# Optimization experiments

Hardware: AMD Instinct MI355X
Metric: run time of the kernel (lower is better)

Reference implementation:

```python
import jax, jax.numpy as jnp
import numpy as np

B, S, H = 8, 2048, 768

def setup_inputs() -> dict:
    key = jax.random.key(0)
    ks = jax.random.split(key, 11)
    queries = jax.random.normal(ks[0], (B, S, H), dtype=jnp.float32)
    keys_ = jax.random.normal(ks[1], (B, S, H), dtype=jnp.float32)
    values = jax.random.normal(ks[2], (B, S, H), dtype=jnp.float32)
    coordinates = jax.random.uniform(ks[3], (B, S, 2), dtype=jnp.float32)
    scale = 1.0 / np.sqrt(H)
    Wq = jax.random.normal(ks[4], (H, H), dtype=jnp.float32) * scale
    bq = jnp.zeros((H,), dtype=jnp.float32)
    Wk = jax.random.normal(ks[5], (H, H), dtype=jnp.float32) * scale
    bk = jnp.zeros((H,), dtype=jnp.float32)
    Wv = jax.random.normal(ks[6], (H, H), dtype=jnp.float32) * scale
    bv = jnp.zeros((H,), dtype=jnp.float32)
    spatial_weight = jax.random.normal(ks[7], (1,), dtype=jnp.float32)
    return {"queries": queries, "keys": keys_, "values": values,
            "coordinates": coordinates, "Wq": Wq, "bq": bq, "Wk": Wk,
            "bk": bk, "Wv": Wv, "bv": bv, "spatial_weight": spatial_weight}

def _cdist(c):
    # c: [B, S, 2] -> pairwise euclidean distances [B, S, S]
    sq = jnp.sum(c * c, axis=-1)  # [B, S]
    d2 = sq[:, :, None] + sq[:, None, :] - 2.0 * jnp.einsum('bsd,btd->bst', c, c)
    return jnp.sqrt(jnp.maximum(d2, 1e-12))

def reference(queries, keys, values, coordinates, Wq, bq, Wk, bk, Wv, bv, spatial_weight):
    q = queries @ Wq.T + bq  # [B, S, H]
    k = keys @ Wk.T + bk
    v = values @ Wv.T + bv
    scores = jnp.einsum('bsh,bth->bst', q, k)          # [B, S, S]
    scores = scores - spatial_weight[0] * _cdist(coordinates)
    attn = jax.nn.softmax(scores, axis=-1)
    out = jnp.einsum('bst,bth->bsh', attn, v)          # [B, S, H]
    return out, attn
```

## Files before the change

kernel.cpp:

```cpp
#include <hip/hip_runtime.h>
#include <stdint.h>


typedef _Float16 half8 __attribute__((ext_vector_type(8)));
typedef _Float16 half4v __attribute__((ext_vector_type(4)));
typedef float f32x4 __attribute__((ext_vector_type(4)));

#define DEVI static __device__ __forceinline__

constexpr int B_ = 8, S_ = 2048, H_ = 768;
constexpr long NX = (long)B_ * S_ * H_;
constexpr long NW = (long)H_ * H_;

DEVI void glds16(const void* g, void* l) {
  __builtin_amdgcn_global_load_lds(
      (const __attribute__((address_space(1))) uint32_t*)g,
      (__attribute__((address_space(3))) uint32_t*)l, 16, 0, 0);
}

DEVI void stage_tile(const _Float16* gbase, int rowStride, _Float16* lds, int tid) {
#pragma unroll
  for (int seg = 0; seg < 2; ++seg) {
    int u = seg * 256 + tid;
    int r = u >> 2, c = u & 3;
    int sc = c ^ ((r >> 1) & 3);
    glds16(gbase + (long)r * rowStride + sc * 8, lds + ((u & ~63) << 3));
  }
}

DEVI half8 frag(const _Float16* lds, int m0, int lane) {
  int row = m0 + (lane & 15);
  int c = (lane >> 4) ^ ((row >> 1) & 3);
  return *(const half8*)(lds + row * 32 + c * 8);
}

__global__ __launch_bounds__(256) void k_split(
    const float* __restrict__ xq, const float* __restrict__ xk,
    const float* __restrict__ xv, const float* __restrict__ wq,
    const float* __restrict__ wk, const float* __restrict__ wv,
    _Float16* __restrict__ dst) {
  const long NX4 = NX / 4, NW4 = NW / 4, TOT = 3 * NX4 + 3 * NW4;
  for (long u = (long)blockIdx.x * blockDim.x + threadIdx.x; u < TOT;
       u += (long)gridDim.x * blockDim.x) {
    const float4* src;
    _Float16 *dh, *dl;
    long idx;
    if (u < 3 * NX4) {
      int z = (u >= 2 * NX4) ? 2 : (u >= NX4) ? 1 : 0;
      idx = u - (long)z * NX4;
      src = (const float4*)(z == 0 ? xq : z == 1 ? xk : xv);
      dh = dst + (long)z * 2 * NX;
      dl = dh + NX;
    } else {
      long t = u - 3 * NX4;
      int z = (t >= 2 * NW4) ? 2 : (t >= NW4) ? 1 : 0;
      idx = t - (long)z * NW4;
      src = (const float4*)(z == 0 ? wq : z == 1 ? wk : wv);
      dh = dst + 6 * NX + (long)z * 2 * NW;
      dl = dh + NW;
    }
    float4 x = src[idx];
    half4v hi, lo;
    hi[0] = (_Float16)x.x; lo[0] = (_Float16)(x.x - (float)hi[0]);
    hi[1] = (_Float16)x.y; lo[1] = (_Float16)(x.y - (float)hi[1]);
    hi[2] = (_Float16)x.z; lo[2] = (_Float16)(x.z - (float)hi[2]);
    hi[3] = (_Float16)x.w; lo[3] = (_Float16)(x.w - (float)hi[3]);
    *(half4v*)(dh + idx * 4) = hi;
    *(half4v*)(dl + idx * 4) = lo;
  }
}

__global__ __launch_bounds__(256, 2) void k_proj(
    const _Float16* __restrict__ scratch, const float* __restrict__ bq,
    const float* __restrict__ bk, const float* __restrict__ bv,
    _Float16* __restrict__ qh, _Float16* __restrict__ ql,
    _Float16* __restrict__ kh, _Float16* __restrict__ kl,
    _Float16* __restrict__ vT) {
  const int nt = blockIdx.x, mt = blockIdx.y, z = blockIdx.z;
  const int tid = threadIdx.x;
  const bool full = (z < 2);
  const _Float16* Xh = scratch + (long)z * 2 * NX;
  const _Float16* Xl = Xh + NX;
  const _Float16* Wh = scratch + 6 * NX + (long)z * 2 * NW;
  const _Float16* Wl = Wh + NW;
  const float* bias = (z == 0) ? bq : (z == 1) ? bk : bv;

  __shared__ _Float16 sm[2][4][4096];

  f32x4 acc[4][4] = {};

  const _Float16* Ah = Xh + (long)(mt * 128) * H_;
  const _Float16* Al = Xl + (long)(mt * 128) * H_;
  const _Float16* Bh = Wh + (long)(nt * 128) * H_;
  const _Float16* Bl = Wl + (long)(nt * 128) * H_;

  stage_tile(Ah, H_, sm[0][0], tid);
  stage_tile(Bh, H_, sm[0][2], tid);
  if (full) {
    stage_tile(Al, H_, sm[0][1], tid);
    stage_tile(Bl, H_, sm[0][3], tid);
  }
  __syncthreads();

  const int lane = tid & 63, wid = tid >> 6;
  const int wm = (wid >> 1) * 64, wn = (wid & 1) * 64;

  int cur = 0;
  for (int kk = 0; kk < 24; ++kk) {
    if (kk + 1 < 24) {
      int o = (kk + 1) * 32;
      stage_tile(Ah + o, H_, sm[cur ^ 1][0], tid);
      stage_tile(Bh + o, H_, sm[cur ^ 1][2], tid);
      if (full) {
        stage_tile(Al + o, H_, sm[cur ^ 1][1], tid);
        stage_tile(Bl + o, H_, sm[cur ^ 1][3], tid);
      }
    }
    half8 ah[4], bh[4];
#pragma unroll
    for (int i = 0; i < 4; ++i) ah[i] = frag(sm[cur][0], wm + i * 16, lane);
#pragma unroll
    for (int j = 0; j < 4; ++j) bh[j] = frag(sm[cur][2], wn + j * 16, lane);
#pragma unroll
    for (int i = 0; i < 4; ++i)
#pragma unroll
      for (int j = 0; j < 4; ++j)
        acc[i][j] = __builtin_amdgcn_mfma_f32_16x16x32_f16(ah[i], bh[j],
                                                           acc[i][j], 0, 0, 0);
    if (full) {
      half8 al[4], bl[4];
#pragma unroll
      for (int i = 0; i < 4; ++i) al[i] = frag(sm[cur][1], wm + i * 16, lane);
#pragma unroll
      for (int j = 0; j < 4; ++j) bl[j] = frag(sm[cur][3], wn + j * 16, lane);
#pragma unroll
      for (int i = 0; i < 4; ++i)
#pragma unroll
        for (int j = 0; j < 4; ++j) {
          acc[i][j] = __builtin_amdgcn_mfma_f32_16x16x32_f16(ah[i], bl[j],
                                                             acc[i][j], 0, 0, 0);
          acc[i][j] = __builtin_amdgcn_mfma_f32_16x16x32_f16(al[i], bh[j],
                                                             acc[i][j], 0, 0, 0);
        }
    }
    __syncthreads();
    cur ^= 1;
  }

  _Float16* oh = (z == 0) ? qh : kh;
  _Float16* ol = (z == 0) ? ql : kl;
#pragma unroll
  for (int i = 0; i < 4; ++i) {
    int m_t = wm + i * 16 + ((lane >> 4) << 2);
#pragma unroll
    for (int j = 0; j < 4; ++j) {
      int n_t = wn + j * 16 + (lane & 15);
      int gn = nt * 128 + n_t;
      float bs = bias[gn];
      if (z < 2) {
#pragma unroll
        for (int r = 0; r < 4; ++r) {
          long gm = (long)mt * 128 + m_t + r;
          float y = acc[i][j][r] + bs;
          _Float16 hi = (_Float16)y;
          oh[gm * H_ + gn] = hi;
          ol[gm * H_ + gn] = (_Float16)(y - (float)hi);
        }
      } else {
        int gmI = mt * 128 + m_t;
        int bb = gmI >> 11, t0 = gmI & 2047;
        half4v pk;
#pragma unroll
        for (int r = 0; r < 4; ++r) pk[r] = (_Float16)(acc[i][j][r] + bs);
        *(half4v*)&vT[((long)bb * H_ + gn) * S_ + t0] = pk;
      }
    }
  }
}

__global__ __launch_bounds__(256, 2) void k_scores(
    const _Float16* __restrict__ qh, const _Float16* __restrict__ ql,
    const _Float16* __restrict__ kh, const _Float16* __restrict__ kl,
    const float* __restrict__ coords, const float* __restrict__ sw,
    float* __restrict__ attn) {
  const int nt = blockIdx.x, mt = blockIdx.y, b = blockIdx.z;
  const int tid = threadIdx.x;
  __shared__ _Float16 sm[2][4][4096];
  __shared__ float cr[2][128], cc[2][128];

  if (tid < 128) {
    long gi = (long)b * S_ + mt * 128 + tid;
    cr[0][tid] = coords[gi * 2 + 0];
    cr[1][tid] = coords[gi * 2 + 1];
  } else {
    int t = tid - 128;
    long gj = (long)b * S_ + nt * 128 + t;
    cc[0][t] = coords[gj * 2 + 0];
    cc[1][t] = coords[gj * 2 + 1];
  }
  const float w = sw[0];

  f32x4 acc[4][4] = {};
  const long aoff = ((long)b * S_ + mt * 128) * H_;
  const long boff = ((long)b * S_ + nt * 128) * H_;
  const _Float16* Ah = qh + aoff;
  const _Float16* Al = ql + aoff;
  const _Float16* Bh = kh + boff;
  const _Float16* Bl = kl + boff;

  stage_tile(Ah, H_, sm[0][0], tid);
  stage_tile(Al, H_, sm[0][1], tid);
  stage_tile(Bh, H_, sm[0][2], tid);
  stage_tile(Bl, H_, sm[0][3], tid);
  __syncthreads();

  const int lane = tid & 63, wid = tid >> 6;
  const int wm = (wid >> 1) * 64, wn = (wid & 1) * 64;

  int cur = 0;
  for (int kk = 0; kk < 24; ++kk) {
    if (kk + 1 < 24) {
      int o = (kk + 1) * 32;
      stage_tile(Ah + o, H_, sm[cur ^ 1][0], tid);
      stage_tile(Al + o, H_, sm[cur ^ 1][1], tid);
      stage_tile(Bh + o, H_, sm[cur ^ 1][2], tid);
      stage_tile(Bl + o, H_, sm[cur ^ 1][3], tid);
    }
    half8 ah[4], al4[4], bh[4], bl4[4];
#pragma unroll
    for (int i = 0; i < 4; ++i) {
      ah[i] = frag(sm[cur][0], wm + i * 16, lane);
      al4[i] = frag(sm[cur][1], wm + i * 16, lane);
    }
#pragma unroll
    for (int j = 0; j < 4; ++j) {
      bh[j] = frag(sm[cur][2], wn + j * 16, lane);
      bl4[j] = frag(sm[cur][3], wn + j * 16, lane);
    }
#pragma unroll
    for (int i = 0; i < 4; ++i)
#pragma unroll
      for (int j = 0; j < 4; ++j) {
        acc[i][j] = __builtin_amdgcn_mfma_f32_16x16x32_f16(ah[i], bh[j],
                                                           acc[i][j], 0, 0, 0);
        acc[i][j] = __builtin_amdgcn_mfma_f32_16x16x32_f16(ah[i], bl4[j],
                                                           acc[i][j], 0, 0, 0);
        acc[i][j] = __builtin_amdgcn_mfma_f32_16x16x32_f16(al4[i], bh[j],
                                                           acc[i][j], 0, 0, 0);
      }
    __syncthreads();
    cur ^= 1;
  }

#pragma unroll
  for (int i = 0; i < 4; ++i) {
    int m_t = wm + i * 16 + ((lane >> 4) << 2);
#pragma unroll
    for (int j = 0; j < 4; ++j) {
      int n_t = wn + j * 16 + (lane & 15);
      float cjx = cc[0][n_t], cjy = cc[1][n_t];
      long rowbase = ((long)b * S_ + mt * 128 + m_t) * S_ + nt * 128 + n_t;
#pragma unroll
      for (int r = 0; r < 4; ++r) {
        float dx = cr[0][m_t + r] - cjx;
        float dy = cr[1][m_t + r] - cjy;
        float d = sqrtf(fmaxf(fmaf(dx, dx, dy * dy), 1e-12f));
        attn[rowbase + (long)r * S_] = acc[i][j][r] - w * d;
      }
    }
  }
}

__global__ __launch_bounds__(256) void k_rowsoft(float* __restrict__ attn) {
  const int wid = threadIdx.x >> 6, lane = threadIdx.x & 63;
  float* p = attn + ((long)blockIdx.x * 4 + wid) * S_;
  float4 v[8];
#pragma unroll
  for (int i = 0; i < 8; ++i) v[i] = ((const float4*)p)[i * 64 + lane];
  float m = -3.4e38f;
#pragma unroll
  for (int i = 0; i < 8; ++i)
    m = fmaxf(m, fmaxf(fmaxf(v[i].x, v[i].y), fmaxf(v[i].z, v[i].w)));
#pragma unroll
  for (int o = 32; o > 0; o >>= 1) m = fmaxf(m, __shfl_xor(m, o));
  float l = 0.f;
#pragma unroll
  for (int i = 0; i < 8; ++i) {
    v[i].x = __expf(v[i].x - m);
    v[i].y = __expf(v[i].y - m);
    v[i].z = __expf(v[i].z - m);
    v[i].w = __expf(v[i].w - m);
    l += (v[i].x + v[i].y) + (v[i].z + v[i].w);
  }
#pragma unroll
  for (int o = 32; o > 0; o >>= 1) l += __shfl_xor(l, o);
  const float rl = 1.0f / l;
#pragma unroll
  for (int i = 0; i < 8; ++i) {
    v[i].x *= rl; v[i].y *= rl; v[i].z *= rl; v[i].w *= rl;
    ((float4*)p)[i * 64 + lane] = v[i];
  }
}

__global__ __launch_bounds__(256, 2) void k_pv(
    const float* __restrict__ attn, const _Float16* __restrict__ vT,
    float* __restrict__ outp) {
  const int nt = blockIdx.x, mt = blockIdx.y, b = blockIdx.z;
  const int tid = threadIdx.x;
  __shared__ _Float16 sm[2][2][4096];
  f32x4 acc[4][4] = {};
  const float* Ab = attn + ((long)b * S_ + mt * 128) * S_;
  const _Float16* Bb = vT + ((long)b * H_ + nt * 128) * S_;
  const int lane = tid & 63, wid = tid >> 6;
  const int wm = (wid >> 1) * 64, wn = (wid & 1) * 64;

  stage_tile(Bb, S_, sm[0][1], tid);
#pragma unroll
  for (int seg = 0; seg < 2; ++seg) {
    int u = seg * 256 + tid, r = u >> 2, c = u & 3;
    int sc = c ^ ((r >> 1) & 3);
    const float4* s4 = (const float4*)(Ab + (long)r * S_ + sc * 8);
    float4 x0 = s4[0], x1 = s4[1];
    half8 h = {(_Float16)x0.x, (_Float16)x0.y, (_Float16)x0.z, (_Float16)x0.w,
               (_Float16)x1.x, (_Float16)x1.y, (_Float16)x1.z, (_Float16)x1.w};
    *(half8*)(&sm[0][0][r * 32 + c * 8]) = h;
  }
  __syncthreads();

  int cur = 0;
  for (int kk = 0; kk < 64; ++kk) {
    float4 x0a, x1a, x0b, x1b;
    const bool pre = (kk + 1 < 64);
    if (pre) {
      stage_tile(Bb + (kk + 1) * 32, S_, sm[cur ^ 1][1], tid);
      {
        int u = tid, r = u >> 2, sc = (u & 3) ^ ((r >> 1) & 3);
        const float4* s4 =
            (const float4*)(Ab + (long)r * S_ + (kk + 1) * 32 + sc * 8);
        x0a = s4[0]; x1a = s4[1];
      }
      {
        int u = 256 + tid, r = u >> 2, sc = (u & 3) ^ ((r >> 1) & 3);
        const float4* s4 =
            (const float4*)(Ab + (long)r * S_ + (kk + 1) * 32 + sc * 8);
        x0b = s4[0]; x1b = s4[1];
      }
    }
    half8 ah[4], bh[4];
#pragma unroll
    for (int i = 0; i < 4; ++i) ah[i] = frag(sm[cur][0], wm + i * 16, lane);
#pragma unroll
    for (int j = 0; j < 4; ++j) bh[j] = frag(sm[cur][1], wn + j * 16, lane);
#pragma unroll
    for (int i = 0; i < 4; ++i)
#pragma unroll
      for (int j = 0; j < 4; ++j)
        acc[i][j] = __builtin_amdgcn_mfma_f32_16x16x32_f16(ah[i], bh[j],
                                                           acc[i][j], 0, 0, 0);
    if (pre) {
      {
        int u = tid, r = u >> 2, c = u & 3;
        half8 h = {(_Float16)x0a.x, (_Float16)x0a.y, (_Float16)x0a.z,
                   (_Float16)x0a.w, (_Float16)x1a.x, (_Float16)x1a.y,
                   (_Float16)x1a.z, (_Float16)x1a.w};
        *(half8*)(&sm[cur ^ 1][0][r * 32 + c * 8]) = h;
      }
      {
        int u = 256 + tid, r = u >> 2, c = u & 3;
        half8 h = {(_Float16)x0b.x, (_Float16)x0b.y, (_Float16)x0b.z,
                   (_Float16)x0b.w, (_Float16)x1b.x, (_Float16)x1b.y,
                   (_Float16)x1b.z, (_Float16)x1b.w};
        *(half8*)(&sm[cur ^ 1][0][r * 32 + c * 8]) = h;
      }
    }
    __syncthreads();
    cur ^= 1;
  }

#pragma unroll
  for (int i = 0; i < 4; ++i) {
    int m_t = wm + i * 16 + ((lane >> 4) << 2);
#pragma unroll
    for (int j = 0; j < 4; ++j) {
      int n_t = wn + j * 16 + (lane & 15);
      int h = nt * 128 + n_t;
      long rowbase = (long)b * S_ + mt * 128 + m_t;
#pragma unroll
      for (int r = 0; r < 4; ++r) outp[(rowbase + r) * H_ + h] = acc[i][j][r];
    }
  }
}

extern "C" void kernel_launch(void* const* d_in, const int* in_sizes, int n_in,
                              void* d_out, int out_size, void* d_ws,
                              size_t ws_size, hipStream_t stream) {
  const float* xq = (const float*)d_in[0];
  const float* xk = (const float*)d_in[1];
  const float* xv = (const float*)d_in[2];
  const float* co = (const float*)d_in[3];
  const float* wq = (const float*)d_in[4];
  const float* bq = (const float*)d_in[5];
  const float* wk = (const float*)d_in[6];
  const float* bk = (const float*)d_in[7];
  const float* wv = (const float*)d_in[8];
  const float* bv = (const float*)d_in[9];
  const float* sw = (const float*)d_in[10];

  float* out = (float*)d_out;
  float* attn = out + NX;
  _Float16* scratch = (_Float16*)d_out;

  _Float16* qh = (_Float16*)d_ws;
  _Float16* ql = qh + NX;
  _Float16* kh = ql + NX;
  _Float16* kl = kh + NX;
  _Float16* vT = kl + NX;

  k_split<<<dim3(2048), 256, 0, stream>>>(xq, xk, xv, wq, wk, wv, scratch);
  k_proj<<<dim3(6, 128, 3), 256, 0, stream>>>(scratch, bq, bk, bv, qh, ql, kh,
                                              kl, vT);
  k_scores<<<dim3(16, 16, 8), 256, 0, stream>>>(qh, ql, kh, kl, co, sw, attn);
  k_rowsoft<<<dim3(4096), 256, 0, stream>>>(attn);
  k_pv<<<dim3(6, 16, 8), 256, 0, stream>>>(attn, vT, out);
}
```

Measured before the change: 557.8 us.

## Rewrite scores GEMM with 256x256 tiles and a 4-stage async LDS pipeline

The QK^T scores kernel now uses 512-thread blocks computing 256x256 output tiles. The three split-precision products (hi*hi, hi*lo, lo*hi) are flattened into one 72-step K loop that stages only two operand tiles per step. A 4-deep ring of LDS buffers is filled with global_load_lds, using swizzled offsets, explicit vmcnt waits and raw barriers, and MFMA runs at raised priority. The aim is more reuse per loaded byte and better overlap of loads with matrix math. The cost is far fewer blocks (512) and heavier register and LDS use per block, which may limit occupancy.

```diff
diff --git a/kernel.cpp b/kernel.cpp
--- a/kernel.cpp
+++ b/kernel.cpp
@@ -178,88 +178,126 @@
   }
 }
 
-__global__ __launch_bounds__(256, 2) void k_scores(
+__global__ __launch_bounds__(512, 2) void k_scores2(
     const _Float16* __restrict__ qh, const _Float16* __restrict__ ql,
     const _Float16* __restrict__ kh, const _Float16* __restrict__ kl,
     const float* __restrict__ coords, const float* __restrict__ sw,
     float* __restrict__ attn) {
   const int nt = blockIdx.x, mt = blockIdx.y, b = blockIdx.z;
   const int tid = threadIdx.x;
-  __shared__ _Float16 sm[2][4][4096];
-  __shared__ float cr[2][128], cc[2][128];
-
-  if (tid < 128) {
-    long gi = (long)b * S_ + mt * 128 + tid;
+  const int lane = tid & 63, wid = tid >> 6;
+  const int wr = wid >> 2, wc = wid & 3;
+
+  __shared__ _Float16 lds[4][2][8192];
+  __shared__ float cr[2][256], cc[2][256];
+
+  if (tid < 256) {
+    long gi = (long)b * S_ + mt * 256 + tid;
     cr[0][tid] = coords[gi * 2 + 0];
     cr[1][tid] = coords[gi * 2 + 1];
   } else {
-    int t = tid - 128;
-    long gj = (long)b * S_ + nt * 128 + t;
+    int t = tid - 256;
+    long gj = (long)b * S_ + nt * 256 + t;
     cc[0][t] = coords[gj * 2 + 0];
     cc[1][t] = coords[gj * 2 + 1];
   }
   const float w = sw[0];
 
-  f32x4 acc[4][4] = {};
-  const long aoff = ((long)b * S_ + mt * 128) * H_;
-  const long boff = ((long)b * S_ + nt * 128) * H_;
-  const _Float16* Ah = qh + aoff;
-  const _Float16* Al = ql + aoff;
-  const _Float16* Bh = kh + boff;
-  const _Float16* Bl = kl + boff;
-
-  stage_tile(Ah, H_, sm[0][0], tid);
-  stage_tile(Al, H_, sm[0][1], tid);
-  stage_tile(Bh, H_, sm[0][2], tid);
-  stage_tile(Bl, H_, sm[0][3], tid);
-  __syncthreads();
-
-  const int lane = tid & 63, wid = tid >> 6;
-  const int wm = (wid >> 1) * 64, wn = (wid & 1) * 64;
-
-  int cur = 0;
-  for (int kk = 0; kk < 24; ++kk) {
-    if (kk + 1 < 24) {
-      int o = (kk + 1) * 32;
-      stage_tile(Ah + o, H_, sm[cur ^ 1][0], tid);
-      stage_tile(Al + o, H_, sm[cur ^ 1][1], tid);
-      stage_tile(Bh + o, H_, sm[cur ^ 1][2], tid);
-      stage_tile(Bl + o, H_, sm[cur ^ 1][3], tid);
-    }
-    half8 ah[4], al4[4], bh[4], bl4[4];
-#pragma unroll
-    for (int i = 0; i < 4; ++i) {
-      ah[i] = frag(sm[cur][0], wm + i * 16, lane);
-      al4[i] = frag(sm[cur][1], wm + i * 16, lane);
-    }
+  const long aoff = ((long)b * S_ + mt * 256) * H_;
+  const long boff = ((long)b * S_ + nt * 256) * H_;
+
+  long goff[2];
+  int loff[2];
+#pragma unroll
+  for (int seg = 0; seg < 2; ++seg) {
+    int u = seg * 512 + tid;
+    int r = u >> 2, c = u & 3;
+    int sc = c ^ ((r >> 1) & 3);
+    goff[seg] = (long)r * H_ + sc * 8;
+    loff[seg] = (u & ~63) << 3;
+  }
+
+  f32x4 acc[8][4] = {};
+
+  auto asrc = [&](int kt) -> const _Float16* {
+    int term = kt / 24, ko = (kt % 24) * 32;
+    return (term == 2 ? ql : qh) + aoff + ko;
+  };
+  auto bsrc = [&](int kt) -> const _Float16* {
+    int term = kt / 24, ko = (kt % 24) * 32;
+    return (term == 1 ? kl : kh) + boff + ko;
+  };
+  auto stage_tile4 = [&](int kt) {
+    const _Float16* sa = asrc(kt);
+    const _Float16* sb = bsrc(kt);
+    _Float16* la = &lds[kt & 3][0][0];
+    _Float16* lb = &lds[kt & 3][1][0];
+    glds16(sa + goff[0], la + loff[0]);
+    glds16(sa + goff[1], la + loff[1]);
+    glds16(sb + goff[0], lb + loff[0]);
+    glds16(sb + goff[1], lb + loff[1]);
+  };
+
+  auto compute = [&](int kt, const _Float16* sa, const _Float16* sb, bool st) {
+    const _Float16* A = &lds[kt & 3][0][0];
+    const _Float16* Bt = &lds[kt & 3][1][0];
+    _Float16* nla = &lds[(kt + 3) & 3][0][0];
+    _Float16* nlb = &lds[(kt + 3) & 3][1][0];
+#pragma unroll
+    for (int q = 0; q < 4; ++q) {
+      const int mh = q >> 1, nh = q & 1;
+      if (st) {
+        int seg = q & 1;
+        if (q < 2)
+          glds16(sa + goff[seg], nla + loff[seg]);
+        else
+          glds16(sb + goff[seg], nlb + loff[seg]);
+      }
+      half8 af[4], bf[2];
+#pragma unroll
+      for (int i = 0; i < 4; ++i)
+        af[i] = frag(A, wr * 128 + (mh * 4 + i) * 16, lane);
+#pragma unroll
+      for (int j = 0; j < 2; ++j)
+        bf[j] = frag(Bt, wc * 64 + (nh * 2 + j) * 16, lane);
+      __builtin_amdgcn_s_setprio(1);
+#pragma unroll
+      for (int i = 0; i < 4; ++i)
+#pragma unroll
+        for (int j = 0; j < 2; ++j)
+          acc[mh * 4 + i][nh * 2 + j] = __builtin_amdgcn_mfma_f32_16x16x32_f16(
+              af[i], bf[j], acc[mh * 4 + i][nh * 2 + j], 0, 0, 0);
+      __builtin_amdgcn_s_setprio(0);
+    }
+  };
+
+  stage_tile4(0);
+  stage_tile4(1);
+  stage_tile4(2);
+  asm volatile("s_waitcnt vmcnt(8)" ::: "memory");
+  __builtin_amdgcn_s_barrier();
+
+  for (int kt = 0; kt < 69; ++kt) {
+    compute(kt, asrc(kt + 3), bsrc(kt + 3), true);
+    asm volatile("s_waitcnt vmcnt(8)" ::: "memory");
+    __builtin_amdgcn_s_barrier();
+  }
+  compute(69, nullptr, nullptr, false);
+  asm volatile("s_waitcnt vmcnt(4)" ::: "memory");
+  __builtin_amdgcn_s_barrier();
+  compute(70, nullptr, nullptr, false);
+  asm volatile("s_waitcnt vmcnt(0)" ::: "memory");
+  __builtin_amdgcn_s_barrier();
+  compute(71, nullptr, nullptr, false);
+
+#pragma unroll
+  for (int i = 0; i < 8; ++i) {
+    int m_t = wr * 128 + i * 16 + ((lane >> 4) << 2);
 #pragma unroll
     for (int j = 0; j < 4; ++j) {
-      bh[j] = frag(sm[cur][2], wn + j * 16, lane);
-      bl4[j] = frag(sm[cur][3], wn + j * 16, lane);
-    }
-#pragma unroll
-    for (int i = 0; i < 4; ++i)
-#pragma unroll
-      for (int j = 0; j < 4; ++j) {
-        acc[i][j] = __builtin_amdgcn_mfma_f32_16x16x32_f16(ah[i], bh[j],
-                                                           acc[i][j], 0, 0, 0);
-        acc[i][j] = __builtin_amdgcn_mfma_f32_16x16x32_f16(ah[i], bl4[j],
-                                                           acc[i][j], 0, 0, 0);
-        acc[i][j] = __builtin_amdgcn_mfma_f32_16x16x32_f16(al4[i], bh[j],
-                                                           acc[i][j], 0, 0, 0);
-      }
-    __syncthreads();
-    cur ^= 1;
-  }
-
-#pragma unroll
-  for (int i = 0; i < 4; ++i) {
-    int m_t = wm + i * 16 + ((lane >> 4) << 2);
-#pragma unroll
-    for (int j = 0; j < 4; ++j) {
-      int n_t = wn + j * 16 + (lane & 15);
+      int n_t = wc * 64 + j * 16 + (lane & 15);
       float cjx = cc[0][n_t], cjy = cc[1][n_t];
-      long rowbase = ((long)b * S_ + mt * 128 + m_t) * S_ + nt * 128 + n_t;
+      long rowbase = ((long)b * S_ + mt * 256 + m_t) * S_ + nt * 256 + n_t;
 #pragma unroll
       for (int r = 0; r < 4; ++r) {
         float dx = cr[0][m_t + r] - cjx;
@@ -419,7 +457,7 @@
   k_split<<<dim3(2048), 256, 0, stream>>>(xq, xk, xv, wq, wk, wv, scratch);
   k_proj<<<dim3(6, 128, 3), 256, 0, stream>>>(scratch, bq, bk, bv, qh, ql, kh,
                                               kl, vT);
-  k_scores<<<dim3(16, 16, 8), 256, 0, stream>>>(qh, ql, kh, kl, co, sw, attn);
+  k_scores2<<<dim3(8, 8, 8), 512, 0, stream>>>(qh, ql, kh, kl, co, sw, attn);
   k_rowsoft<<<dim3(4096), 256, 0, stream>>>(attn);
   k_pv<<<dim3(6, 16, 8), 256, 0, stream>>>(attn, vT, out);
 }
```

New measurement: 616.3 us. 10.5% more time.

## Fold Wq and Wk into one matrix so only one activation projection is needed

Applied to the files above, without the earlier changes.

Rewrites the scores as (Xq·(Wq^T Wk))·Xk^T plus rank-one bias terms. A small GEMM builds G = Wq^T Wk, only Xq is projected by it, and the raw Xk is used directly as the key operand. This drops one full 16K×768×768 split-precision projection. The per-row and per-column bias corrections are added in the scores epilogue. The value projection now runs straight from fp32 in its own kernel. Softmax also writes an fp16 copy of the attention matrix so the PV GEMM can stage it with direct global-to-LDS loads. The cost is extra small kernels, a 2048×2048×8 fp16 write, and numerical drift from the reassociated product.

```diff
diff --git a/kernel.cpp b/kernel.cpp
--- a/kernel.cpp
+++ b/kernel.cpp
@@ -11,6 +11,7 @@
 constexpr int B_ = 8, S_ = 2048, H_ = 768;
 constexpr long NX = (long)B_ * S_ * H_;
 constexpr long NW = (long)H_ * H_;
+constexpr long ATT = (long)B_ * S_ * S_;
 
 DEVI void glds16(const void* g, void* l) {
   __builtin_amdgcn_global_load_lds(
@@ -34,30 +35,49 @@
   return *(const half8*)(lds + row * 32 + c * 8);
 }
 
+__global__ __launch_bounds__(128) void k_uv(const float* __restrict__ wq,
+                                            const float* __restrict__ wk,
+                                            const float* __restrict__ bq,
+                                            const float* __restrict__ bk,
+                                            float* u, float* vv, float* cb) {
+  int i = blockIdx.x * 128 + threadIdx.x;
+  if (blockIdx.y == 0) {
+    float a = 0;
+    for (int j = 0; j < H_; ++j) a += wq[(long)j * H_ + i] * bk[j];
+    u[i] = a;
+    if (i == 0) {
+      float c = 0;
+      for (int j = 0; j < H_; ++j) c += bq[j] * bk[j];
+      cb[0] = c;
+    }
+  } else {
+    float a = 0;
+    for (int j = 0; j < H_; ++j) a += wk[(long)j * H_ + i] * bq[j];
+    vv[i] = a;
+  }
+}
+
 __global__ __launch_bounds__(256) void k_split(
     const float* __restrict__ xq, const float* __restrict__ xk,
-    const float* __restrict__ xv, const float* __restrict__ wq,
-    const float* __restrict__ wk, const float* __restrict__ wv,
-    _Float16* __restrict__ dst) {
-  const long NX4 = NX / 4, NW4 = NW / 4, TOT = 3 * NX4 + 3 * NW4;
-  for (long u = (long)blockIdx.x * blockDim.x + threadIdx.x; u < TOT;
-       u += (long)gridDim.x * blockDim.x) {
+    const float* __restrict__ wq, const float* __restrict__ wk,
+    _Float16* __restrict__ xh, _Float16* __restrict__ xl,
+    _Float16* __restrict__ yh, _Float16* __restrict__ yl,
+    _Float16* __restrict__ wqh, _Float16* __restrict__ wql,
+    _Float16* __restrict__ wkh, _Float16* __restrict__ wkl) {
+  const long NX4 = NX / 4, NW4 = NW / 4, TOT = 2 * NX4 + 2 * NW4;
+  for (long t = (long)blockIdx.x * blockDim.x + threadIdx.x; t < TOT;
+       t += (long)gridDim.x * blockDim.x) {
     const float4* src;
     _Float16 *dh, *dl;
     long idx;
-    if (u < 3 * NX4) {
-      int z = (u >= 2 * NX4) ? 2 : (u >= NX4) ? 1 : 0;
-      idx = u - (long)z * NX4;
-      src = (const float4*)(z == 0 ? xq : z == 1 ? xk : xv);
-      dh = dst + (long)z * 2 * NX;
-      dl = dh + NX;
+    if (t < NX4) {
+      src = (const float4*)xq; dh = xh; dl = xl; idx = t;
+    } else if (t < 2 * NX4) {
+      src = (const float4*)xk; dh = yh; dl = yl; idx = t - NX4;
     } else {
-      long t = u - 3 * NX4;
-      int z = (t >= 2 * NW4) ? 2 : (t >= NW4) ? 1 : 0;
-      idx = t - (long)z * NW4;
-      src = (const float4*)(z == 0 ? wq : z == 1 ? wk : wv);
-      dh = dst + 6 * NX + (long)z * 2 * NW;
-      dl = dh + NW;
+      long v = t - 2 * NX4;
+      if (v < NW4) { src = (const float4*)wq; dh = wqh; dl = wql; idx = v; }
+      else { src = (const float4*)wk; dh = wkh; dl = wkl; idx = v - NW4; }
     }
     float4 x = src[idx];
     half4v hi, lo;
@@ -70,36 +90,67 @@
   }
 }
 
-__global__ __launch_bounds__(256, 2) void k_proj(
-    const _Float16* __restrict__ scratch, const float* __restrict__ bq,
-    const float* __restrict__ bk, const float* __restrict__ bv,
-    _Float16* __restrict__ qh, _Float16* __restrict__ ql,
-    _Float16* __restrict__ kh, _Float16* __restrict__ kl,
-    _Float16* __restrict__ vT) {
-  const int nt = blockIdx.x, mt = blockIdx.y, z = blockIdx.z;
+__global__ __launch_bounds__(256) void k_tr(const _Float16* __restrict__ in,
+                                            _Float16* __restrict__ out) {
+  const int z = blockIdx.z;
+  const _Float16* src = in + (long)z * NW;
+  _Float16* dst = out + (long)z * NW;
+  __shared__ _Float16 t[64][72];
+  int r0 = blockIdx.y * 64, c0 = blockIdx.x * 64;
+#pragma unroll
+  for (int it = 0; it < 2; ++it) {
+    int idx = it * 256 + threadIdx.x;
+    int r = idx >> 3, ch = idx & 7;
+    *(half8*)&t[r][ch * 8] = *(const half8*)(src + (long)(r0 + r) * H_ + c0 + ch * 8);
+  }
+  __syncthreads();
+#pragma unroll
+  for (int it = 0; it < 2; ++it) {
+    int idx = it * 256 + threadIdx.x;
+    int r = idx >> 3, ch = idx & 7;
+    half8 v;
+#pragma unroll
+    for (int k = 0; k < 8; ++k) v[k] = t[ch * 8 + k][r];
+    *(half8*)(dst + (long)(c0 + r) * H_ + r0 + ch * 8) = v;
+  }
+}
+
+__global__ __launch_bounds__(256) void k_dot(const float* __restrict__ src,
+                                             const float* __restrict__ vec,
+                                             const float* __restrict__ cb,
+                                             float* __restrict__ dst, int addc) {
+  int wid = threadIdx.x >> 6, lane = threadIdx.x & 63;
+  long row = (long)blockIdx.x * 4 + wid;
+  const float4* p = (const float4*)(src + row * H_);
+  const float4* q = (const float4*)vec;
+  float s = 0;
+#pragma unroll
+  for (int k = 0; k < 3; ++k) {
+    float4 a = p[lane + k * 64], b = q[lane + k * 64];
+    s += a.x * b.x + a.y * b.y + a.z * b.z + a.w * b.w;
+  }
+#pragma unroll
+  for (int o = 32; o; o >>= 1) s += __shfl_xor(s, o);
+  if (lane == 0) dst[row] = s + (addc ? cb[0] : 0.0f);
+}
+
+__global__ __launch_bounds__(256, 2) void k_gemm3(
+    const _Float16* __restrict__ Ah_, const _Float16* __restrict__ Al_,
+    const _Float16* __restrict__ Bh_, const _Float16* __restrict__ Bl_,
+    _Float16* __restrict__ Oh, _Float16* __restrict__ Ol) {
+  const int nt = blockIdx.x, mt = blockIdx.y;
   const int tid = threadIdx.x;
-  const bool full = (z < 2);
-  const _Float16* Xh = scratch + (long)z * 2 * NX;
-  const _Float16* Xl = Xh + NX;
-  const _Float16* Wh = scratch + 6 * NX + (long)z * 2 * NW;
-  const _Float16* Wl = Wh + NW;
-  const float* bias = (z == 0) ? bq : (z == 1) ? bk : bv;
-
   __shared__ _Float16 sm[2][4][4096];
-
   f32x4 acc[4][4] = {};
-
-  const _Float16* Ah = Xh + (long)(mt * 128) * H_;
-  const _Float16* Al = Xl + (long)(mt * 128) * H_;
-  const _Float16* Bh = Wh + (long)(nt * 128) * H_;
-  const _Float16* Bl = Wl + (long)(nt * 128) * H_;
+  const _Float16* Ah = Ah_ + (long)(mt * 128) * H_;
+  const _Float16* Al = Al_ + (long)(mt * 128) * H_;
+  const _Float16* Bh = Bh_ + (long)(nt * 128) * H_;
+  const _Float16* Bl = Bl_ + (long)(nt * 128) * H_;
 
   stage_tile(Ah, H_, sm[0][0], tid);
   stage_tile(Bh, H_, sm[0][2], tid);
-  if (full) {
-    stage_tile(Al, H_, sm[0][1], tid);
-    stage_tile(Bl, H_, sm[0][3], tid);
-  }
+  stage_tile(Al, H_, sm[0][1], tid);
+  stage_tile(Bl, H_, sm[0][3], tid);
   __syncthreads();
 
   const int lane = tid & 63, wid = tid >> 6;
@@ -111,44 +162,35 @@
       int o = (kk + 1) * 32;
       stage_tile(Ah + o, H_, sm[cur ^ 1][0], tid);
       stage_tile(Bh + o, H_, sm[cur ^ 1][2], tid);
-      if (full) {
-        stage_tile(Al + o, H_, sm[cur ^ 1][1], tid);
-        stage_tile(Bl + o, H_, sm[cur ^ 1][3], tid);
+      stage_tile(Al + o, H_, sm[cur ^ 1][1], tid);
+      stage_tile(Bl + o, H_, sm[cur ^ 1][3], tid);
+    }
+    half8 ah[4], bh[4], al[4], bl[4];
+#pragma unroll
+    for (int i = 0; i < 4; ++i) {
+      ah[i] = frag(sm[cur][0], wm + i * 16, lane);
+      al[i] = frag(sm[cur][1], wm + i * 16, lane);
+    }
+#pragma unroll
+    for (int j = 0; j < 4; ++j) {
+      bh[j] = frag(sm[cur][2], wn + j * 16, lane);
+      bl[j] = frag(sm[cur][3], wn + j * 16, lane);
+    }
+#pragma unroll
+    for (int i = 0; i < 4; ++i)
+#pragma unroll
+      for (int j = 0; j < 4; ++j) {
+        acc[i][j] = __builtin_amdgcn_mfma_f32_16x16x32_f16(ah[i], bh[j],
+                                                           acc[i][j], 0, 0, 0);
+        acc[i][j] = __builtin_amdgcn_mfma_f32_16x16x32_f16(ah[i], bl[j],
+                                                           acc[i][j], 0, 0, 0);
+        acc[i][j] = __builtin_amdgcn_mfma_f32_16x16x32_f16(al[i], bh[j],
+                                                           acc[i][j], 0, 0, 0);
       }
-    }
-    half8 ah[4], bh[4];
-#pragma unroll
-    for (int i = 0; i < 4; ++i) ah[i] = frag(sm[cur][0], wm + i * 16, lane);
-#pragma unroll
-    for (int j = 0; j < 4; ++j) bh[j] = frag(sm[cur][2], wn + j * 16, lane);
-#pragma unroll
-    for (int i = 0; i < 4; ++i)
-#pragma unroll
-      for (int j = 0; j < 4; ++j)
-        acc[i][j] = __builtin_amdgcn_mfma_f32_16x16x32_f16(ah[i], bh[j],
-                                                           acc[i][j], 0, 0, 0);
-    if (full) {
-      half8 al[4], bl[4];
-#pragma unroll
-      for (int i = 0; i < 4; ++i) al[i] = frag(sm[cur][1], wm + i * 16, lane);
-#pragma unroll
-      for (int j = 0; j < 4; ++j) bl[j] = frag(sm[cur][3], wn + j * 16, lane);
-#pragma unroll
-      for (int i = 0; i < 4; ++i)
-#pragma unroll
-        for (int j = 0; j < 4; ++j) {
-          acc[i][j] = __builtin_amdgcn_mfma_f32_16x16x32_f16(ah[i], bl[j],
-                                                             acc[i][j], 0, 0, 0);
-          acc[i][j] = __builtin_amdgcn_mfma_f32_16x16x32_f16(al[i], bh[j],
-                                                             acc[i][j], 0, 0, 0);
-        }
-    }
     __syncthreads();
     cur ^= 1;
   }
 
-  _Float16* oh = (z == 0) ? qh : kh;
-  _Float16* ol = (z == 0) ? ql : kl;
 #pragma unroll
   for (int i = 0; i < 4; ++i) {
     int m_t = wm + i * 16 + ((lane >> 4) << 2);
@@ -156,57 +198,50 @@
     for (int j = 0; j < 4; ++j) {
       int n_t = wn + j * 16 + (lane & 15);
       int gn = nt * 128 + n_t;
-      float bs = bias[gn];
-      if (z < 2) {
-#pragma unroll
-        for (int r = 0; r < 4; ++r) {
-          long gm = (long)mt * 128 + m_t + r;
-          float y = acc[i][j][r] + bs;
-          _Float16 hi = (_Float16)y;
-          oh[gm * H_ + gn] = hi;
-          ol[gm * H_ + gn] = (_Float16)(y - (float)hi);
-        }
-      } else {
-        int gmI = mt * 128 + m_t;
-        int bb = gmI >> 11, t0 = gmI & 2047;
-        half4v pk;
-#pragma unroll
-        for (int r = 0; r < 4; ++r) pk[r] = (_Float16)(acc[i][j][r] + bs);
-        *(half4v*)&vT[((long)bb * H_ + gn) * S_ + t0] = pk;
+#pragma unroll
+      for (int r = 0; r < 4; ++r) {
+        long gm = (long)mt * 128 + m_t + r;
+        float y = acc[i][j][r];
+        _Float16 hi = (_Float16)y;
+        Oh[gm * H_ + gn] = hi;
+        Ol[gm * H_ + gn] = (_Float16)(y - (float)hi);
       }
     }
   }
 }
 
 __global__ __launch_bounds__(256, 2) void k_scores(
-    const _Float16* __restrict__ qh, const _Float16* __restrict__ ql,
-    const _Float16* __restrict__ kh, const _Float16* __restrict__ kl,
+    const _Float16* __restrict__ ph, const _Float16* __restrict__ pl,
+    const _Float16* __restrict__ yh, const _Float16* __restrict__ yl,
     const float* __restrict__ coords, const float* __restrict__ sw,
+    const float* __restrict__ rowadd, const float* __restrict__ coladd,
     float* __restrict__ attn) {
   const int nt = blockIdx.x, mt = blockIdx.y, b = blockIdx.z;
   const int tid = threadIdx.x;
   __shared__ _Float16 sm[2][4][4096];
-  __shared__ float cr[2][128], cc[2][128];
+  __shared__ float cr[2][128], cc[2][128], ra[128], ca[128];
 
   if (tid < 128) {
     long gi = (long)b * S_ + mt * 128 + tid;
     cr[0][tid] = coords[gi * 2 + 0];
     cr[1][tid] = coords[gi * 2 + 1];
+    ra[tid] = rowadd[gi];
   } else {
     int t = tid - 128;
     long gj = (long)b * S_ + nt * 128 + t;
     cc[0][t] = coords[gj * 2 + 0];
     cc[1][t] = coords[gj * 2 + 1];
+    ca[t] = coladd[gj];
   }
   const float w = sw[0];
 
   f32x4 acc[4][4] = {};
   const long aoff = ((long)b * S_ + mt * 128) * H_;
   const long boff = ((long)b * S_ + nt * 128) * H_;
-  const _Float16* Ah = qh + aoff;
-  const _Float16* Al = ql + aoff;
-  const _Float16* Bh = kh + boff;
-  const _Float16* Bl = kl + boff;
+  const _Float16* Ah = ph + aoff;
+  const _Float16* Al = pl + aoff;
+  const _Float16* Bh = yh + boff;
+  const _Float16* Bl = yl + boff;
 
   stage_tile(Ah, H_, sm[0][0], tid);
   stage_tile(Al, H_, sm[0][1], tid);
@@ -265,15 +300,18 @@
         float dx = cr[0][m_t + r] - cjx;
         float dy = cr[1][m_t + r] - cjy;
         float d = sqrtf(fmaxf(fmaf(dx, dx, dy * dy), 1e-12f));
-        attn[rowbase + (long)r * S_] = acc[i][j][r] - w * d;
+        attn[rowbase + (long)r * S_] = acc[i][j][r] - w * d + ra[m_t + r] + ca[n_t];
       }
     }
   }
 }
 
-__global__ __launch_bounds__(256) void k_rowsoft(float* __restrict__ attn) {
+__global__ __launch_bounds__(256) void k_rowsoft(float* __restrict__ attn,
+                                                 _Float16* __restrict__ a16) {
   const int wid = threadIdx.x >> 6, lane = threadIdx.x & 63;
-  float* p = attn + ((long)blockIdx.x * 4 + wid) * S_;
+  long row = (long)blockIdx.x * 4 + wid;
+  float* p = attn + row * S_;
+  _Float16* p16 = a16 + row * S_;
   float4 v[8];
 #pragma unroll
   for (int i = 0; i < 8; ++i) v[i] = ((const float4*)p)[i * 64 + lane];
@@ -299,52 +337,122 @@
   for (int i = 0; i < 8; ++i) {
     v[i].x *= rl; v[i].y *= rl; v[i].z *= rl; v[i].w *= rl;
     ((float4*)p)[i * 64 + lane] = v[i];
-  }
-}
-
-__global__ __launch_bounds__(256, 2) void k_pv(
-    const float* __restrict__ attn, const _Float16* __restrict__ vT,
+    half4v h = {(_Float16)v[i].x, (_Float16)v[i].y, (_Float16)v[i].z,
+                (_Float16)v[i].w};
+    ((half4v*)p16)[i * 64 + lane] = h;
+  }
+}
+
+__global__ __launch_bounds__(256, 2) void k_projv(
+    const float* __restrict__ vals, const float* __restrict__ wv,
+    const float* __restrict__ bv, _Float16* __restrict__ vT) {
+  const int nt = blockIdx.x, mt = blockIdx.y;
+  const int tid = threadIdx.x, lane = tid & 63, wid = tid >> 6;
+  const int wm = (wid >> 1) * 64, wn = (wid & 1) * 64;
+  __shared__ _Float16 sm[2][2][4096];
+  f32x4 acc[4][4] = {};
+  const float* Ab = vals + (long)(mt * 128) * H_;
+  const float* Bb = wv + (long)(nt * 128) * H_;
+
+#pragma unroll
+  for (int op = 0; op < 2; ++op) {
+    const float* gb = op ? Bb : Ab;
+#pragma unroll
+    for (int seg = 0; seg < 2; ++seg) {
+      int u = seg * 256 + tid, r = u >> 2, c = u & 3;
+      int sc = c ^ ((r >> 1) & 3);
+      const float4* s4 = (const float4*)(gb + (long)r * H_ + sc * 8);
+      float4 x0 = s4[0], x1 = s4[1];
+      half8 h = {(_Float16)x0.x, (_Float16)x0.y, (_Float16)x0.z, (_Float16)x0.w,
+                 (_Float16)x1.x, (_Float16)x1.y, (_Float16)x1.z, (_Float16)x1.w};
+      *(half8*)(&sm[0][op][r * 32 + c * 8]) = h;
+    }
+  }
+  __syncthreads();
+
+  int cur = 0;
+  for (int kk = 0; kk < 24; ++kk) {
+    float4 pa[2][2], pb[2][2];
+    const bool pre = (kk + 1 < 24);
+    if (pre) {
+#pragma unroll
+      for (int seg = 0; seg < 2; ++seg) {
+        int u = seg * 256 + tid, r = u >> 2;
+        int sc = (u & 3) ^ ((r >> 1) & 3);
+        const float4* s4 = (const float4*)(Ab + (long)r * H_ + (kk + 1) * 32 + sc * 8);
+        pa[seg][0] = s4[0]; pa[seg][1] = s4[1];
+        const float4* t4 = (const float4*)(Bb + (long)r * H_ + (kk + 1) * 32 + sc * 8);
+        pb[seg][0] = t4[0]; pb[seg][1] = t4[1];
+      }
+    }
+    half8 ah[4], bh[4];
+#pragma unroll
+    for (int i = 0; i < 4; ++i) ah[i] = frag(sm[cur][0], wm + i * 16, lane);
+#pragma unroll
+    for (int j = 0; j < 4; ++j) bh[j] = frag(sm[cur][1], wn + j * 16, lane);
+#pragma unroll
+    for (int i = 0; i < 4; ++i)
+#pragma unroll
+      for (int j = 0; j < 4; ++j)
+        acc[i][j] = __builtin_amdgcn_mfma_f32_16x16x32_f16(ah[i], bh[j],
+                                                           acc[i][j], 0, 0, 0);
+    if (pre) {
+#pragma unroll
+      for (int op = 0; op < 2; ++op) {
+#pragma unroll
+        for (int seg = 0; seg < 2; ++seg) {
+          int u = seg * 256 + tid, r = u >> 2, c = u & 3;
+          float4 x0 = op ? pb[seg][0] : pa[seg][0];
+          float4 x1 = op ? pb[seg][1] : pa[seg][1];
+          half8 h = {(_Float16)x0.x, (_Float16)x0.y, (_Float16)x0.z,
+                     (_Float16)x0.w, (_Float16)x1.x, (_Float16)x1.y,
+                     (_Float16)x1.z, (_Float16)x1.w};
+          *(half8*)(&sm[cur ^ 1][op][r * 32 + c * 8]) = h;
+        }
+      }
+    }
+    __syncthreads();
+    cur ^= 1;
+  }
+
+#pragma unroll
+  for (int i = 0; i < 4; ++i) {
+    int m_t = wm + i * 16 + ((lane >> 4) << 2);
+#pragma unroll
+    for (int j = 0; j < 4; ++j) {
+      int n_t = wn + j * 16 + (lane & 15);
+      int gn = nt * 128 + n_t;
+      float bs = bv[gn];
+      int gmI = mt * 128 + m_t;
+      int bb = gmI >> 11, t0 = gmI & 2047;
+      half4v pk;
+#pragma unroll
+      for (int r = 0; r < 4; ++r) pk[r] = (_Float16)(acc[i][j][r] + bs);
+      *(half4v*)&vT[((long)bb * H_ + gn) * S_ + t0] = pk;
+    }
+  }
+}
+
+__global__ __launch_bounds__(256, 2) void k_pv16(
+    const _Float16* __restrict__ a16, const _Float16* __restrict__ vT,
     float* __restrict__ outp) {
   const int nt = blockIdx.x, mt = blockIdx.y, b = blockIdx.z;
-  const int tid = threadIdx.x;
+  const int tid = threadIdx.x, lane = tid & 63, wid = tid >> 6;
+  const int wm = (wid >> 1) * 64, wn = (wid & 1) * 64;
   __shared__ _Float16 sm[2][2][4096];
   f32x4 acc[4][4] = {};
-  const float* Ab = attn + ((long)b * S_ + mt * 128) * S_;
+  const _Float16* Ab = a16 + ((long)b * S_ + mt * 128) * S_;
   const _Float16* Bb = vT + ((long)b * H_ + nt * 128) * S_;
-  const int lane = tid & 63, wid = tid >> 6;
-  const int wm = (wid >> 1) * 64, wn = (wid & 1) * 64;
-
+
+  stage_tile(Ab, S_, sm[0][0], tid);
   stage_tile(Bb, S_, sm[0][1], tid);
-#pragma unroll
-  for (int seg = 0; seg < 2; ++seg) {
-    int u = seg * 256 + tid, r = u >> 2, c = u & 3;
-    int sc = c ^ ((r >> 1) & 3);
-    const float4* s4 = (const float4*)(Ab + (long)r * S_ + sc * 8);
-    float4 x0 = s4[0], x1 = s4[1];
-    half8 h = {(_Float16)x0.x, (_Float16)x0.y, (_Float16)x0.z, (_Float16)x0.w,
-               (_Float16)x1.x, (_Float16)x1.y, (_Float16)x1.z, (_Float16)x1.w};
-    *(half8*)(&sm[0][0][r * 32 + c * 8]) = h;
-  }
   __syncthreads();
 
   int cur = 0;
   for (int kk = 0; kk < 64; ++kk) {
-    float4 x0a, x1a, x0b, x1b;
-    const bool pre = (kk + 1 < 64);
-    if (pre) {
+    if (kk + 1 < 64) {
+      stage_tile(Ab + (kk + 1) * 32, S_, sm[cur ^ 1][0], tid);
       stage_tile(Bb + (kk + 1) * 32, S_, sm[cur ^ 1][1], tid);
-      {
-        int u = tid, r = u >> 2, sc = (u & 3) ^ ((r >> 1) & 3);
-        const float4* s4 =
-            (const float4*)(Ab + (long)r * S_ + (kk + 1) * 32 + sc * 8);
-        x0a = s4[0]; x1a = s4[1];
-      }
-      {
-        int u = 256 + tid, r = u >> 2, sc = (u & 3) ^ ((r >> 1) & 3);
-        const float4* s4 =
-            (const float4*)(Ab + (long)r * S_ + (kk + 1) * 32 + sc * 8);
-        x0b = s4[0]; x1b = s4[1];
-      }
     }
     half8 ah[4], bh[4];
 #pragma unroll
@@ -357,22 +465,6 @@
       for (int j = 0; j < 4; ++j)
         acc[i][j] = __builtin_amdgcn_mfma_f32_16x16x32_f16(ah[i], bh[j],
                                                            acc[i][j], 0, 0, 0);
-    if (pre) {
-      {
-        int u = tid, r = u >> 2, c = u & 3;
-        half8 h = {(_Float16)x0a.x, (_Float16)x0a.y, (_Float16)x0a.z,
-                   (_Float16)x0a.w, (_Float16)x1a.x, (_Float16)x1a.y,
-                   (_Float16)x1a.z, (_Float16)x1a.w};
-        *(half8*)(&sm[cur ^ 1][0][r * 32 + c * 8]) = h;
-      }
-      {
-        int u = 256 + tid, r = u >> 2, c = u & 3;
-        half8 h = {(_Float16)x0b.x, (_Float16)x0b.y, (_Float16)x0b.z,
-                   (_Float16)x0b.w, (_Float16)x1b.x, (_Float16)x1b.y,
-                   (_Float16)x1b.z, (_Float16)x1b.w};
-        *(half8*)(&sm[cur ^ 1][0][r * 32 + c * 8]) = h;
-      }
-    }
     __syncthreads();
     cur ^= 1;
   }
@@ -408,18 +500,41 @@
 
   float* out = (float*)d_out;
   float* attn = out + NX;
-  _Float16* scratch = (_Float16*)d_out;
-
-  _Float16* qh = (_Float16*)d_ws;
-  _Float16* ql = qh + NX;
-  _Float16* kh = ql + NX;
-  _Float16* kl = kh + NX;
-  _Float16* vT = kl + NX;
-
-  k_split<<<dim3(2048), 256, 0, stream>>>(xq, xk, xv, wq, wk, wv, scratch);
-  k_proj<<<dim3(6, 128, 3), 256, 0, stream>>>(scratch, bq, bk, bv, qh, ql, kh,
-                                              kl, vT);
-  k_scores<<<dim3(16, 16, 8), 256, 0, stream>>>(qh, ql, kh, kl, co, sw, attn);
-  k_rowsoft<<<dim3(4096), 256, 0, stream>>>(attn);
-  k_pv<<<dim3(6, 16, 8), 256, 0, stream>>>(attn, vT, out);
-}
+
+  _Float16* sc = (_Float16*)d_out;
+  _Float16* Xh = sc;
+  _Float16* Xl = sc + NX;
+  _Float16* Wbase = sc + 2 * NX;
+  _Float16* WT = Wbase + 4 * NW;
+  _Float16* GtH = Wbase + 8 * NW;
+  _Float16* GtL = GtH + NW;
+
+  _Float16* wsh = (_Float16*)d_ws;
+  _Float16* Ph = wsh;
+  _Float16* Pl = wsh + NX;
+  _Float16* Yh = wsh + 2 * NX;
+  _Float16* Yl = wsh + 3 * NX;
+  float* extras = (float*)(wsh + 4 * NX);
+  float* rowadd = extras;
+  float* coladd = extras + 16384;
+  float* u = extras + 32768;
+  float* vv = u + H_;
+  float* cb = vv + H_;
+  _Float16* a16 = wsh;
+  _Float16* vT = wsh + ATT;
+
+  k_uv<<<dim3(6, 2), 128, 0, stream>>>(wq, wk, bq, bk, u, vv, cb);
+  k_split<<<2048, 256, 0, stream>>>(xq, xk, wq, wk, Xh, Xl, Yh, Yl, Wbase,
+                                    Wbase + NW, Wbase + 2 * NW, Wbase + 3 * NW);
+  k_tr<<<dim3(12, 12, 4), 256, 0, stream>>>(Wbase, WT);
+  k_gemm3<<<dim3(6, 6), 256, 0, stream>>>(WT + 2 * NW, WT + 3 * NW, WT,
+                                          WT + NW, GtH, GtL);
+  k_dot<<<4096, 256, 0, stream>>>(xq, u, cb, rowadd, 1);
+  k_dot<<<4096, 256, 0, stream>>>(xk, vv, cb, coladd, 0);
+  k_gemm3<<<dim3(6, 128), 256, 0, stream>>>(Xh, Xl, GtH, GtL, Ph, Pl);
+  k_scores<<<dim3(16, 16, 8), 256, 0, stream>>>(Ph, Pl, Yh, Yl, co, sw, rowadd,
+                                                coladd, attn);
+  k_rowsoft<<<4096, 256, 0, stream>>>(attn, a16);
+  k_projv<<<dim3(6, 128), 256, 0, stream>>>(xv, wv, bv, vT);
+  k_pv16<<<dim3(6, 16, 8), 256, 0, stream>>>(a16, vT, out);
+}
```

Result: slower. 641.7 us (+15.0%).
